# Optimization experiments

Hardware: AMD Instinct MI355X
Metric: run time of the kernel (lower is better)

The kernel has to match this reference:

```python
import jax, jax.numpy as jnp
import numpy as np

B, S, D_MODEL, HEADS, DK = 2, 2048, 1024, 16, 64


def setup_inputs() -> dict:
    key = jax.random.key(0)
    ks = jax.random.split(key, 7)
    scale = 0.02
    return {
        "query": jax.random.normal(ks[0], (B, S, D_MODEL), jnp.float32),
        "key": jax.random.normal(ks[1], (B, S, D_MODEL), jnp.float32),
        "value": jax.random.normal(ks[2], (B, S, D_MODEL), jnp.float32),
        "Wq": jax.random.normal(ks[3], (D_MODEL, HEADS * DK), jnp.float32) * scale,
        "bq": jax.random.normal(ks[4], (HEADS * DK,), jnp.float32) * scale,
        "Wo": jax.random.normal(ks[5], (HEADS * DK, D_MODEL), jnp.float32) * scale,
        "bo": jax.random.normal(ks[6], (D_MODEL,), jnp.float32) * scale,
    }


def reference(query, key, value, Wq, bq, Wo, bo):
    # NOTE: faithful to the original code, which (buggily) uses _W_q to
    # project query, key AND value, and scales by sqrt(seq_len), not sqrt(d_k).
    seq_len = key.shape[1]

    def split_heads(x):
        # [B,S,H*DK] -> [H,B,S,DK]; torch chunk(dim=-1)+cat(dim=0) stacks head h
        # (slice h*DK:(h+1)*DK) at batch block h.
        p = x @ Wq + bq
        b, s, _ = p.shape
        return p.reshape(b, s, HEADS, DK).transpose(2, 0, 1, 3)

    q = split_heads(query)   # [H,B,S,DK]
    k = split_heads(key)
    v = split_heads(value)

    inv_scale = jnp.float32(1.0 / np.sqrt(seq_len))
    scores = jnp.einsum("hbqd,hbkd->hbqk", q, k) * inv_scale  # [H,B,S,S]
    attn = jax.nn.softmax(scores, axis=-1)
    out = jnp.einsum("hbqk,hbkd->hbqd", attn, v)  # [H,B,S,DK]
    # inverse of chunk(dim=0)+cat(dim=-1): [H,B,S,DK] -> [B,S,H*DK]
    out = out.transpose(1, 2, 0, 3).reshape(query.shape[0], query.shape[1], HEADS * DK)
    return out @ Wo + bo
```

## Files before the change

### kernel.cpp

```cpp
#include <hip/hip_runtime.h>

#define DEVI __device__ __forceinline__

typedef short short4_t __attribute__((ext_vector_type(4)));
typedef short short8_t __attribute__((ext_vector_type(8)));
typedef __bf16 bf16x8 __attribute__((ext_vector_type(8)));
typedef float f32x4 __attribute__((ext_vector_type(4)));

DEVI short f2bf(float f) {
    union { float f; unsigned u; } v; v.f = f;
    unsigned r = (v.u + 0x7fffu + ((v.u >> 16) & 1u)) >> 16;
    return (short)r;
}

DEVI unsigned pack_ru(float a, float b) {
    union { float f; unsigned u; } x, y; x.f = a; y.f = b;
    return __builtin_amdgcn_perm(y.u + 0x8000u, x.u + 0x8000u, 0x07060302u);
}

DEVI void g2lds16(const short* g, short* l) {
    __builtin_amdgcn_global_load_lds(
        (const __attribute__((address_space(1))) void*)g,
        (__attribute__((address_space(3))) void*)l, 16, 0, 0);
}

__global__ __launch_bounds__(256) void cvt3_kernel(const float* __restrict__ q,
                                                   const float* __restrict__ k,
                                                   const float* __restrict__ v,
                                                   short* __restrict__ X) {
    const size_t N1 = (size_t)4096 * 1024;
    size_t e = ((size_t)blockIdx.x * 256 + threadIdx.x) * 4;
    const float* src; size_t off;
    if (e < N1)            { src = q; off = e; }
    else if (e < 2 * N1)   { src = k; off = e - N1; }
    else                   { src = v; off = e - 2 * N1; }
    f32x4 f = *(const f32x4*)(src + off);
    short4_t o;
    o[0] = f2bf(f[0]); o[1] = f2bf(f[1]); o[2] = f2bf(f[2]); o[3] = f2bf(f[3]);
    *(short4_t*)(X + e) = o;
}

__global__ __launch_bounds__(256) void transpose_w_kernel(const float* __restrict__ W,
                                                          short* __restrict__ Wt) {
    __shared__ short T[64][65];
    const int t = threadIdx.x;
    const int kt = blockIdx.x * 64, nt = blockIdx.y * 64;
#pragma unroll
    for (int r = 0; r < 4; ++r) {
        int kl = (t >> 4) + 16 * r;
        int n0 = (t & 15) * 4;
        f32x4 f = *(const f32x4*)(W + (size_t)(kt + kl) * 1024 + nt + n0);
#pragma unroll
        for (int j = 0; j < 4; ++j) T[n0 + j][kl] = f2bf(f[j]);
    }
    __syncthreads();
#pragma unroll
    for (int r = 0; r < 2; ++r) {
        int nl = (t >> 3) + 32 * r;
        int k0 = (t & 7) * 8;
        short8_t v;
#pragma unroll
        for (int j = 0; j < 8; ++j) v[j] = T[nl][k0 + j];
        *(short8_t*)(Wt + (size_t)(nt + nl) * 1024 + kt + k0) = v;
    }
}

template <typename OutT>
__global__ __launch_bounds__(256) void gemm_bt_kernel(const short* __restrict__ A,
                                                      const short* __restrict__ Bt,
                                                      const float* __restrict__ bias,
                                                      OutT* __restrict__ C,
                                                      int M, int N, int K,
                                                      int qrows, float qscale) {
    __shared__ __align__(16) short As[128 * 32];
    __shared__ __align__(16) short Bs[128 * 32];
    const int tid  = threadIdx.x;
    const int lane = tid & 63, wave = tid >> 6;
    const int quad = lane >> 4, l16 = lane & 15;
    const int row0 = blockIdx.x * 128, col0 = blockIdx.y * 128;
    const int wm = (wave >> 1) * 64, wn = (wave & 1) * 64;
    const int srow = lane >> 2;
    const int scol = (lane & 3) * 8;
    f32x4 acc[4][4] = {};
    for (int k0 = 0; k0 < K; k0 += 32) {
#pragma unroll
        for (int r = 0; r < 2; ++r) {
            int rb = r * 64 + wave * 16;
            g2lds16(A  + (size_t)(row0 + rb + srow) * K + k0 + scol, &As[rb * 32]);
            g2lds16(Bt + (size_t)(col0 + rb + srow) * K + k0 + scol, &Bs[rb * 32]);
        }
        __syncthreads();
        bf16x8 af[4], bfr[4];
#pragma unroll
        for (int mi = 0; mi < 4; ++mi) af[mi]  = *(const bf16x8*)&As[(wm + mi * 16 + l16) * 32 + quad * 8];
#pragma unroll
        for (int ni = 0; ni < 4; ++ni) bfr[ni] = *(const bf16x8*)&Bs[(wn + ni * 16 + l16) * 32 + quad * 8];
#pragma unroll
        for (int mi = 0; mi < 4; ++mi)
#pragma unroll
            for (int ni = 0; ni < 4; ++ni)
                acc[mi][ni] = __builtin_amdgcn_mfma_f32_16x16x32_bf16(af[mi], bfr[ni], acc[mi][ni], 0, 0, 0);
        __syncthreads();
    }
#pragma unroll
    for (int mi = 0; mi < 4; ++mi) {
#pragma unroll
        for (int ni = 0; ni < 4; ++ni) {
            int col = col0 + wn + ni * 16 + l16;
            float bv = bias[col];
#pragma unroll
            for (int i = 0; i < 4; ++i) {
                int row = row0 + wm + mi * 16 + quad * 4 + i;
                float val = acc[mi][ni][i] + bv;
                if (row < qrows) val *= qscale;
                if constexpr (sizeof(OutT) == 2) C[(size_t)row * N + col] = (OutT)f2bf(val);
                else                             C[(size_t)row * N + col] = (OutT)val;
            }
        }
    }
}

__global__ __launch_bounds__(256) void gemm_bt64_kernel(const short* __restrict__ A,
                                                        const short* __restrict__ Bt,
                                                        const float* __restrict__ bias,
                                                        float* __restrict__ C,
                                                        int M, int N, int K) {
    __shared__ __align__(16) short As[64 * 32];
    __shared__ __align__(16) short Bs[128 * 32];
    const int tid  = threadIdx.x;
    const int lane = tid & 63, wave = tid >> 6;
    const int quad = lane >> 4, l16 = lane & 15;
    const int row0 = blockIdx.x * 64, col0 = blockIdx.y * 128;
    const int wn = wave * 32;
    const int srow = lane >> 2;
    const int scol = (lane & 3) * 8;
    f32x4 acc[4][2] = {};
    for (int k0 = 0; k0 < K; k0 += 32) {
        {
            int rb = wave * 16;
            g2lds16(A + (size_t)(row0 + rb + srow) * K + k0 + scol, &As[rb * 32]);
        }
#pragma unroll
        for (int r = 0; r < 2; ++r) {
            int rb = r * 64 + wave * 16;
            g2lds16(Bt + (size_t)(col0 + rb + srow) * K + k0 + scol, &Bs[rb * 32]);
        }
        __syncthreads();
        bf16x8 af[4], bfr[2];
#pragma unroll
        for (int mi = 0; mi < 4; ++mi) af[mi]  = *(const bf16x8*)&As[(mi * 16 + l16) * 32 + quad * 8];
#pragma unroll
        for (int ni = 0; ni < 2; ++ni) bfr[ni] = *(const bf16x8*)&Bs[(wn + ni * 16 + l16) * 32 + quad * 8];
#pragma unroll
        for (int mi = 0; mi < 4; ++mi)
#pragma unroll
            for (int ni = 0; ni < 2; ++ni)
                acc[mi][ni] = __builtin_amdgcn_mfma_f32_16x16x32_bf16(af[mi], bfr[ni], acc[mi][ni], 0, 0, 0);
        __syncthreads();
    }
#pragma unroll
    for (int mi = 0; mi < 4; ++mi) {
#pragma unroll
        for (int ni = 0; ni < 2; ++ni) {
            int col = col0 + wn + ni * 16 + l16;
            float bv = bias[col];
#pragma unroll
            for (int i = 0; i < 4; ++i) {
                int row = row0 + mi * 16 + quad * 4 + i;
                C[(size_t)row * N + col] = acc[mi][ni][i] + bv;
            }
        }
    }
}

__global__ __launch_bounds__(256) void transpose_v_kernel(const short* __restrict__ Pv,
                                                          short* __restrict__ VT) {
    __shared__ short T[64][65];
    const int t = threadIdx.x;
    const int hb = blockIdx.x, st = blockIdx.y * 64;
    const int h = hb >> 1, b = hb & 1;
#pragma unroll
    for (int r = 0; r < 2; ++r) {
        int sl = (t >> 3) + 32 * r;
        short8_t v = *(const short8_t*)(Pv + (size_t)(b * 2048 + st + sl) * 1024 + h * 64 + (t & 7) * 8);
#pragma unroll
        for (int j = 0; j < 8; ++j) T[(t & 7) * 8 + j][sl] = v[j];
    }
    __syncthreads();
#pragma unroll
    for (int r = 0; r < 2; ++r) {
        int dl = (t >> 3) + 32 * r;
        short8_t v;
#pragma unroll
        for (int j = 0; j < 8; ++j) v[j] = T[dl][(t & 7) * 8 + j];
        *(short8_t*)(VT + ((size_t)hb * 64 + dl) * 2048 + st + (t & 7) * 8) = v;
    }
}

__global__ __launch_bounds__(256, 2) void attn_kernel(const short* __restrict__ P,
                                                      const short* __restrict__ VT,
                                                      short* __restrict__ O) {
    constexpr int LDK = 72;
    constexpr int LDV = 136;
    constexpr int LDO = 72;
    union SmemU {
        struct { short Ks[2][128 * LDK]; short Vs[2][64 * LDV]; } s;
        short OT[128 * LDO];
    };
    __shared__ __align__(16) SmemU sm;

    const int t = threadIdx.x;
    const int lane = t & 63, wave = t >> 6;
    const int quad = lane >> 4, l16 = lane & 15;
    const int bx = blockIdx.x;
    const int xcd = bx & 7, bi = bx >> 3;
    const int hb = xcd * 4 + (bi & 3), qt = bi >> 2;
    const int h = hb >> 1, b = hb & 1;
    const short* Pq  = P + (size_t)(b * 2048 + qt * 128) * 1024 + h * 64;
    const short* Pk  = P + (size_t)(4096 + b * 2048) * 1024 + h * 64;
    const short* VTh = VT + (size_t)hb * 64 * 2048;
    const int wq = wave * 32;

    bf16x8 qf[2][2];
#pragma unroll
    for (int miq = 0; miq < 2; ++miq)
#pragma unroll
        for (int kh = 0; kh < 2; ++kh)
            qf[miq][kh] = *(const bf16x8*)(Pq + (size_t)(wq + miq * 16 + l16) * 1024 + kh * 32 + quad * 8);

    bf16x8 ones;
#pragma unroll
    for (int j = 0; j < 8; ++j) ones[j] = (__bf16)1.0f;

    f32x4 oacc[4][2] = {};
    f32x4 osum[2] = {};

    const int krow = t >> 3, kc8 = (t & 7) * 8;
    const int kj = krow & 7, kq = krow >> 3;
    const int lrow32 = (kj >= 4 ? 16 + (kj - 4) : kj) + kq * 4;
    const int vrow = t >> 4, vc8 = (t & 15) * 8;

    short8_t kreg[4], vreg[4];
#pragma unroll
    for (int it = 0; it < 4; ++it) {
        kreg[it] = *(const short8_t*)(Pk + (size_t)(it * 32 + krow) * 1024 + kc8);
        vreg[it] = *(const short8_t*)(VTh + (size_t)(it * 16 + vrow) * 2048 + vc8);
    }

    for (int tile = 0; tile < 16; ++tile) {
        const int buf = tile & 1;
        short* Ksb = sm.s.Ks[buf];
        short* Vsb = sm.s.Vs[buf];
#pragma unroll
        for (int it = 0; it < 4; ++it) {
            *(short8_t*)&Ksb[(it * 32 + lrow32) * LDK + kc8] = kreg[it];
            *(short8_t*)&Vsb[(it * 16 + vrow) * LDV + vc8] = vreg[it];
        }
        __syncthreads();
        if (tile + 1 < 16) {
            int kv0 = (tile + 1) * 128;
#pragma unroll
            for (int it = 0; it < 4; ++it) {
                kreg[it] = *(const short8_t*)(Pk + (size_t)(kv0 + it * 32 + krow) * 1024 + kc8);
                vreg[it] = *(const short8_t*)(VTh + (size_t)(it * 16 + vrow) * 2048 + kv0 + vc8);
            }
        }
#pragma unroll
        for (int p = 0; p < 4; ++p) {
            bf16x8 aA0 = *(const bf16x8*)&Ksb[(p * 32 + l16) * LDK + quad * 8];
            bf16x8 aA1 = *(const bf16x8*)&Ksb[(p * 32 + l16) * LDK + 32 + quad * 8];
            bf16x8 aB0 = *(const bf16x8*)&Ksb[(p * 32 + 16 + l16) * LDK + quad * 8];
            bf16x8 aB1 = *(const bf16x8*)&Ksb[(p * 32 + 16 + l16) * LDK + 32 + quad * 8];
            bf16x8 vA[4];
#pragma unroll
            for (int di = 0; di < 4; ++di)
                vA[di] = *(const bf16x8*)&Vsb[(di * 16 + l16) * LDV + p * 32 + quad * 8];
#pragma unroll
            for (int miq = 0; miq < 2; ++miq) {
                f32x4 sA = {}, sB = {};
                sA = __builtin_amdgcn_mfma_f32_16x16x32_bf16(aA0, qf[miq][0], sA, 0, 0, 0);
                sB = __builtin_amdgcn_mfma_f32_16x16x32_bf16(aB0, qf[miq][0], sB, 0, 0, 0);
                sA = __builtin_amdgcn_mfma_f32_16x16x32_bf16(aA1, qf[miq][1], sA, 0, 0, 0);
                sB = __builtin_amdgcn_mfma_f32_16x16x32_bf16(aB1, qf[miq][1], sB, 0, 0, 0);
                float eA0 = __builtin_amdgcn_exp2f(sA[0]);
                float eA1 = __builtin_amdgcn_exp2f(sA[1]);
                float eA2 = __builtin_amdgcn_exp2f(sA[2]);
                float eA3 = __builtin_amdgcn_exp2f(sA[3]);
                float eB0 = __builtin_amdgcn_exp2f(sB[0]);
                float eB1 = __builtin_amdgcn_exp2f(sB[1]);
                float eB2 = __builtin_amdgcn_exp2f(sB[2]);
                float eB3 = __builtin_amdgcn_exp2f(sB[3]);
                union { unsigned u[4]; bf16x8 b8; } pb;
                pb.u[0] = pack_ru(eA0, eA1);
                pb.u[1] = pack_ru(eA2, eA3);
                pb.u[2] = pack_ru(eB0, eB1);
                pb.u[3] = pack_ru(eB2, eB3);
                osum[miq] = __builtin_amdgcn_mfma_f32_16x16x32_bf16(ones, pb.b8, osum[miq], 0, 0, 0);
#pragma unroll
                for (int di = 0; di < 4; ++di)
                    oacc[di][miq] = __builtin_amdgcn_mfma_f32_16x16x32_bf16(vA[di], pb.b8, oacc[di][miq], 0, 0, 0);
            }
        }
    }

    float rinv[2];
#pragma unroll
    for (int miq = 0; miq < 2; ++miq) rinv[miq] = 1.0f / osum[miq][0];

    __syncthreads();

#pragma unroll
    for (int di = 0; di < 4; ++di) {
#pragma unroll
        for (int miq = 0; miq < 2; ++miq) {
            float v0 = oacc[di][miq][0] * rinv[miq];
            float v1 = oacc[di][miq][1] * rinv[miq];
            float v2 = oacc[di][miq][2] * rinv[miq];
            float v3 = oacc[di][miq][3] * rinv[miq];
            uint2 w;
            w.x = pack_ru(v0, v1);
            w.y = pack_ru(v2, v3);
            int q = wq + miq * 16 + l16;
            *(uint2*)&sm.OT[q * LDO + di * 16 + quad * 4] = w;
        }
    }
    __syncthreads();
    {
        const int orow = t >> 1, ocol = (t & 1) * 32;
        short* dst = O + (size_t)(b * 2048 + qt * 128 + orow) * 1024 + h * 64 + ocol;
#pragma unroll
        for (int c = 0; c < 4; ++c)
            *(short8_t*)(dst + c * 8) = *(const short8_t*)&sm.OT[orow * LDO + ocol + c * 8];
    }
}

extern "C" void kernel_launch(void* const* d_in, const int* in_sizes, int n_in,
                              void* d_out, int out_size, void* d_ws, size_t ws_size,
                              hipStream_t stream) {
    (void)in_sizes; (void)n_in; (void)out_size; (void)ws_size;
    const float* q  = (const float*)d_in[0];
    const float* k  = (const float*)d_in[1];
    const float* v  = (const float*)d_in[2];
    const float* Wq = (const float*)d_in[3];
    const float* bq = (const float*)d_in[4];
    const float* Wo = (const float*)d_in[5];
    const float* bo = (const float*)d_in[6];
    float* out = (float*)d_out;

    short* Xcat = (short*)d_ws;
    short* WqT  = Xcat + (size_t)12288 * 1024;
    short* WoT  = WqT + (size_t)1024 * 1024;
    short* P    = WoT + (size_t)1024 * 1024;
    short* VT   = P + (size_t)12288 * 1024;
    short* O    = VT + (size_t)32 * 64 * 2048;

    const float qscale = 0.022097086912079608f * 1.4426950408889634f;

    cvt3_kernel<<<12288, 256, 0, stream>>>(q, k, v, Xcat);
    transpose_w_kernel<<<dim3(16, 16), 256, 0, stream>>>(Wq, WqT);
    transpose_w_kernel<<<dim3(16, 16), 256, 0, stream>>>(Wo, WoT);
    gemm_bt_kernel<short><<<dim3(96, 8), 256, 0, stream>>>(Xcat, WqT, bq, P, 12288, 1024, 1024, 4096, qscale);
    transpose_v_kernel<<<dim3(32, 32), 256, 0, stream>>>(P + (size_t)8192 * 1024, VT);
    attn_kernel<<<512, 256, 0, stream>>>(P, VT, O);
    gemm_bt64_kernel<<<dim3(64, 8), 256, 0, stream>>>(O, WoT, bo, out, 4096, 1024, 1024);
}
```

Before: 214.6 us.

## Split KV range across wave pairs in attention kernel and merge partials via LDS

```diff
diff --git a/kernel.cpp b/kernel.cpp
--- a/kernel.cpp
+++ b/kernel.cpp
@@ -203,9 +203,10 @@
     constexpr int LDK = 72;
     constexpr int LDV = 136;
     constexpr int LDO = 72;
+    constexpr int LDF = 68;
     union SmemU {
         struct { short Ks[2][128 * LDK]; short Vs[2][64 * LDV]; } s;
-        short OT[128 * LDO];
+        struct { float Of[2][64 * LDF]; float Osum[2][64]; short OT[128 * LDO]; } r;
     };
     __shared__ __align__(16) SmemU sm;
 
@@ -219,11 +220,14 @@
     const short* Pq  = P + (size_t)(b * 2048 + qt * 128) * 1024 + h * 64;
     const short* Pk  = P + (size_t)(4096 + b * 2048) * 1024 + h * 64;
     const short* VTh = VT + (size_t)hb * 64 * 2048;
-    const int wq = wave * 32;
-
-    bf16x8 qf[2][2];
-#pragma unroll
-    for (int miq = 0; miq < 2; ++miq)
+
+    const int sb = wave >> 1;
+    const int wq = (wave & 1) * 64;
+    const int ts = t & 127;
+
+    bf16x8 qf[4][2];
+#pragma unroll
+    for (int miq = 0; miq < 4; ++miq)
 #pragma unroll
         for (int kh = 0; kh < 2; ++kh)
             qf[miq][kh] = *(const bf16x8*)(Pq + (size_t)(wq + miq * 16 + l16) * 1024 + kh * 32 + quad * 8);
@@ -232,37 +236,39 @@
 #pragma unroll
     for (int j = 0; j < 8; ++j) ones[j] = (__bf16)1.0f;
 
-    f32x4 oacc[4][2] = {};
-    f32x4 osum[2] = {};
-
-    const int krow = t >> 3, kc8 = (t & 7) * 8;
-    const int kj = krow & 7, kq = krow >> 3;
-    const int lrow32 = (kj >= 4 ? 16 + (kj - 4) : kj) + kq * 4;
-    const int vrow = t >> 4, vc8 = (t & 15) * 8;
-
-    short8_t kreg[4], vreg[4];
-#pragma unroll
-    for (int it = 0; it < 4; ++it) {
-        kreg[it] = *(const short8_t*)(Pk + (size_t)(it * 32 + krow) * 1024 + kc8);
-        vreg[it] = *(const short8_t*)(VTh + (size_t)(it * 16 + vrow) * 2048 + vc8);
-    }
-
-    for (int tile = 0; tile < 16; ++tile) {
-        const int buf = tile & 1;
-        short* Ksb = sm.s.Ks[buf];
-        short* Vsb = sm.s.Vs[buf];
-#pragma unroll
-        for (int it = 0; it < 4; ++it) {
-            *(short8_t*)&Ksb[(it * 32 + lrow32) * LDK + kc8] = kreg[it];
-            *(short8_t*)&Vsb[(it * 16 + vrow) * LDV + vc8] = vreg[it];
-        }
-        __syncthreads();
-        if (tile + 1 < 16) {
-            int kv0 = (tile + 1) * 128;
-#pragma unroll
-            for (int it = 0; it < 4; ++it) {
-                kreg[it] = *(const short8_t*)(Pk + (size_t)(kv0 + it * 32 + krow) * 1024 + kc8);
-                vreg[it] = *(const short8_t*)(VTh + (size_t)(it * 16 + vrow) * 2048 + kv0 + vc8);
+    f32x4 oacc[4][4] = {};
+    f32x4 osum[4] = {};
+
+    const int krow16 = ts >> 3, kc8 = (ts & 7) * 8;
+    const int vrow8 = ts >> 4, vc8 = (ts & 15) * 8;
+
+    const size_t kvbase = (size_t)sb * 1024;
+    short8_t kreg[8], vreg[8];
+#pragma unroll
+    for (int it = 0; it < 8; ++it) {
+        kreg[it] = *(const short8_t*)(Pk + (kvbase + it * 16 + krow16) * 1024 + kc8);
+        vreg[it] = *(const short8_t*)(VTh + (size_t)(it * 8 + vrow8) * 2048 + kvbase + vc8);
+    }
+
+    short* Ksb = sm.s.Ks[sb];
+    short* Vsb = sm.s.Vs[sb];
+
+    for (int tile = 0; tile < 8; ++tile) {
+#pragma unroll
+        for (int it = 0; it < 8; ++it) {
+            int w32 = ((it & 1) << 4) + krow16;
+            int kj = w32 & 7, kq = w32 >> 3;
+            int lr = (it >> 1) * 32 + (kj >= 4 ? 16 + (kj - 4) : kj) + kq * 4;
+            *(short8_t*)&Ksb[lr * LDK + kc8] = kreg[it];
+            *(short8_t*)&Vsb[(it * 8 + vrow8) * LDV + vc8] = vreg[it];
+        }
+        __syncthreads();
+        if (tile + 1 < 8) {
+            size_t kv0 = kvbase + (size_t)(tile + 1) * 128;
+#pragma unroll
+            for (int it = 0; it < 8; ++it) {
+                kreg[it] = *(const short8_t*)(Pk + (kv0 + it * 16 + krow16) * 1024 + kc8);
+                vreg[it] = *(const short8_t*)(VTh + (size_t)(it * 8 + vrow8) * 2048 + kv0 + vc8);
             }
         }
 #pragma unroll
@@ -276,7 +282,7 @@
             for (int di = 0; di < 4; ++di)
                 vA[di] = *(const bf16x8*)&Vsb[(di * 16 + l16) * LDV + p * 32 + quad * 8];
 #pragma unroll
-            for (int miq = 0; miq < 2; ++miq) {
+            for (int miq = 0; miq < 4; ++miq) {
                 f32x4 sA = {}, sB = {};
                 sA = __builtin_amdgcn_mfma_f32_16x16x32_bf16(aA0, qf[miq][0], sA, 0, 0, 0);
                 sB = __builtin_amdgcn_mfma_f32_16x16x32_bf16(aB0, qf[miq][0], sB, 0, 0, 0);
@@ -301,27 +307,43 @@
                     oacc[di][miq] = __builtin_amdgcn_mfma_f32_16x16x32_bf16(vA[di], pb.b8, oacc[di][miq], 0, 0, 0);
             }
         }
-    }
-
-    float rinv[2];
-#pragma unroll
-    for (int miq = 0; miq < 2; ++miq) rinv[miq] = 1.0f / osum[miq][0];
-
+        __syncthreads();
+    }
+
+    const int wv = wave & 1;
+    if (sb == 1) {
+#pragma unroll
+        for (int di = 0; di < 4; ++di)
+#pragma unroll
+            for (int miq = 0; miq < 4; ++miq)
+                *(f32x4*)&sm.r.Of[wv][(miq * 16 + l16) * LDF + di * 16 + quad * 4] = oacc[di][miq];
+        if (quad == 0) {
+#pragma unroll
+            for (int miq = 0; miq < 4; ++miq)
+                sm.r.Osum[wv][miq * 16 + l16] = osum[miq][0];
+        }
+    }
     __syncthreads();
-
-#pragma unroll
-    for (int di = 0; di < 4; ++di) {
-#pragma unroll
-        for (int miq = 0; miq < 2; ++miq) {
-            float v0 = oacc[di][miq][0] * rinv[miq];
-            float v1 = oacc[di][miq][1] * rinv[miq];
-            float v2 = oacc[di][miq][2] * rinv[miq];
-            float v3 = oacc[di][miq][3] * rinv[miq];
-            uint2 w;
-            w.x = pack_ru(v0, v1);
-            w.y = pack_ru(v2, v3);
-            int q = wq + miq * 16 + l16;
-            *(uint2*)&sm.OT[q * LDO + di * 16 + quad * 4] = w;
+    if (sb == 0) {
+        float rinv[4];
+#pragma unroll
+        for (int miq = 0; miq < 4; ++miq)
+            rinv[miq] = 1.0f / (osum[miq][0] + sm.r.Osum[wv][miq * 16 + l16]);
+#pragma unroll
+        for (int di = 0; di < 4; ++di) {
+#pragma unroll
+            for (int miq = 0; miq < 4; ++miq) {
+                f32x4 ob = *(const f32x4*)&sm.r.Of[wv][(miq * 16 + l16) * LDF + di * 16 + quad * 4];
+                float v0 = (oacc[di][miq][0] + ob[0]) * rinv[miq];
+                float v1 = (oacc[di][miq][1] + ob[1]) * rinv[miq];
+                float v2 = (oacc[di][miq][2] + ob[2]) * rinv[miq];
+                float v3 = (oacc[di][miq][3] + ob[3]) * rinv[miq];
+                uint2 w;
+                w.x = pack_ru(v0, v1);
+                w.y = pack_ru(v2, v3);
+                int q = wq + miq * 16 + l16;
+                *(uint2*)&sm.r.OT[q * LDO + di * 16 + quad * 4] = w;
+            }
         }
     }
     __syncthreads();
@@ -330,7 +352,7 @@
         short* dst = O + (size_t)(b * 2048 + qt * 128 + orow) * 1024 + h * 64 + ocol;
 #pragma unroll
         for (int c = 0; c < 4; ++c)
-            *(short8_t*)(dst + c * 8) = *(const short8_t*)&sm.OT[orow * LDO + ocol + c * 8];
+            *(short8_t*)(dst + c * 8) = *(const short8_t*)&sm.r.OT[orow * LDO + ocol + c * 8];
     }
 }
 
```

Result: slower. 237.8 us (+10.8%).

## Load V fragments directly from global into registers, dropping V LDS staging

Applied to the files above, without the earlier changes.

```diff
diff --git a/kernel.cpp b/kernel.cpp
--- a/kernel.cpp
+++ b/kernel.cpp
@@ -201,10 +201,9 @@
                                                       const short* __restrict__ VT,
                                                       short* __restrict__ O) {
     constexpr int LDK = 72;
-    constexpr int LDV = 136;
     constexpr int LDO = 72;
     union SmemU {
-        struct { short Ks[2][128 * LDK]; short Vs[2][64 * LDV]; } s;
+        short Ks[2][128 * LDK];
         short OT[128 * LDO];
     };
     __shared__ __align__(16) SmemU sm;
@@ -238,43 +237,46 @@
     const int krow = t >> 3, kc8 = (t & 7) * 8;
     const int kj = krow & 7, kq = krow >> 3;
     const int lrow32 = (kj >= 4 ? 16 + (kj - 4) : kj) + kq * 4;
-    const int vrow = t >> 4, vc8 = (t & 15) * 8;
-
-    short8_t kreg[4], vreg[4];
-#pragma unroll
-    for (int it = 0; it < 4; ++it) {
+
+    short8_t kreg[4];
+#pragma unroll
+    for (int it = 0; it < 4; ++it)
         kreg[it] = *(const short8_t*)(Pk + (size_t)(it * 32 + krow) * 1024 + kc8);
-        vreg[it] = *(const short8_t*)(VTh + (size_t)(it * 16 + vrow) * 2048 + vc8);
-    }
+
+    const short* Vg = VTh + (size_t)l16 * 2048 + quad * 8;
+    bf16x8 vA[2][4];
+#pragma unroll
+    for (int di = 0; di < 4; ++di)
+        vA[0][di] = *(const bf16x8*)(Vg + (size_t)di * 16 * 2048);
 
     for (int tile = 0; tile < 16; ++tile) {
         const int buf = tile & 1;
-        short* Ksb = sm.s.Ks[buf];
-        short* Vsb = sm.s.Vs[buf];
-#pragma unroll
-        for (int it = 0; it < 4; ++it) {
+        short* Ksb = sm.Ks[buf];
+#pragma unroll
+        for (int it = 0; it < 4; ++it)
             *(short8_t*)&Ksb[(it * 32 + lrow32) * LDK + kc8] = kreg[it];
-            *(short8_t*)&Vsb[(it * 16 + vrow) * LDV + vc8] = vreg[it];
-        }
         __syncthreads();
         if (tile + 1 < 16) {
             int kv0 = (tile + 1) * 128;
 #pragma unroll
-            for (int it = 0; it < 4; ++it) {
+            for (int it = 0; it < 4; ++it)
                 kreg[it] = *(const short8_t*)(Pk + (size_t)(kv0 + it * 32 + krow) * 1024 + kc8);
-                vreg[it] = *(const short8_t*)(VTh + (size_t)(it * 16 + vrow) * 2048 + kv0 + vc8);
+        }
+#pragma unroll
+        for (int p = 0; p < 4; ++p) {
+            const int pp = p & 1;
+            {
+                const int ntile = (p == 3) ? ((tile + 1) & 15) : tile;
+                const int np = (p + 1) & 3;
+                const int ncol = ntile * 128 + np * 32;
+#pragma unroll
+                for (int di = 0; di < 4; ++di)
+                    vA[pp ^ 1][di] = *(const bf16x8*)(Vg + (size_t)di * 16 * 2048 + ncol);
             }
-        }
-#pragma unroll
-        for (int p = 0; p < 4; ++p) {
             bf16x8 aA0 = *(const bf16x8*)&Ksb[(p * 32 + l16) * LDK + quad * 8];
             bf16x8 aA1 = *(const bf16x8*)&Ksb[(p * 32 + l16) * LDK + 32 + quad * 8];
             bf16x8 aB0 = *(const bf16x8*)&Ksb[(p * 32 + 16 + l16) * LDK + quad * 8];
             bf16x8 aB1 = *(const bf16x8*)&Ksb[(p * 32 + 16 + l16) * LDK + 32 + quad * 8];
-            bf16x8 vA[4];
-#pragma unroll
-            for (int di = 0; di < 4; ++di)
-                vA[di] = *(const bf16x8*)&Vsb[(di * 16 + l16) * LDV + p * 32 + quad * 8];
 #pragma unroll
             for (int miq = 0; miq < 2; ++miq) {
                 f32x4 sA = {}, sB = {};
@@ -298,7 +300,7 @@
                 osum[miq] = __builtin_amdgcn_mfma_f32_16x16x32_bf16(ones, pb.b8, osum[miq], 0, 0, 0);
 #pragma unroll
                 for (int di = 0; di < 4; ++di)
-                    oacc[di][miq] = __builtin_amdgcn_mfma_f32_16x16x32_bf16(vA[di], pb.b8, oacc[di][miq], 0, 0, 0);
+                    oacc[di][miq] = __builtin_amdgcn_mfma_f32_16x16x32_bf16(vA[pp][di], pb.b8, oacc[di][miq], 0, 0, 0);
             }
         }
     }
```

New measurement: 237.4 us. 1.11x slower.
